# Kernel optimization log

Hardware: AMD Instinct MI355X
Metric: run time of the kernel (lower is better)

Reference implementation:

```python
import jax, jax.numpy as jnp
import numpy as np
from jax import lax

DIM = 1024
BATCH = 16
WIDTH = 2048
DECAY = 0.99


def setup_inputs() -> dict:
    key = jax.random.key(0)
    k1, k2, k3, k4 = jax.random.split(key, 4)
    scale = 1.0 / np.sqrt(DIM)
    x = jax.random.normal(k1, (BATCH, WIDTH, DIM), dtype=jnp.float32)
    state = jnp.zeros((BATCH, DIM), dtype=jnp.float32)
    Wv = jax.random.normal(k2, (DIM, DIM), dtype=jnp.float32) * scale
    Wr = jax.random.normal(k3, (DIM, DIM), dtype=jnp.float32) * scale
    Wc = jax.random.normal(k4, (DIM, DIM), dtype=jnp.float32) * scale
    return {"x": x, "state": state, "Wv": Wv, "Wr": Wr, "Wc": Wc}


def reference(x, state, Wv, Wr, Wc):
    # x: [B, W, D], state: [B, D]; fixed-decay RWKV recurrence along width.
    decay = jnp.asarray(DECAY, dtype=x.dtype)
    one_minus = jnp.asarray(1.0, dtype=x.dtype) - decay
    v = jnp.einsum('bwd,de->bwe', x, Wv)                 # value projection
    r = jax.nn.sigmoid(jnp.einsum('bwd,de->bwe', x, Wr))  # receptance

    # scan over width (time) axis: elems shaped [W, B, D]
    def step(s_prev, inp):
        v_t, r_t, x_t = inp
        s_curr = decay * s_prev + one_minus * v_t
        y_t = x_t + r_t * s_curr
        return s_curr, y_t

    elems = (jnp.swapaxes(v, 0, 1), jnp.swapaxes(r, 0, 1), jnp.swapaxes(x, 0, 1))
    new_state, y_t = lax.scan(step, state, elems)
    y = jnp.swapaxes(y_t, 0, 1)                          # [B, W, D]
    y = y + jnp.einsum('bwd,de->bwe', y, Wc)             # minimal channel mix
    return y, new_state
```

## Files before the change

kernel.cpp:

```cpp
#include <hip/hip_runtime.h>
#include <hip/hip_bf16.h>
#include <math.h>


#define MROWS 32768
#define NCHUNK 16
#define CHUNKL 128
#define DECAY_F 0.99f
#define OM_F 0.01f

typedef __attribute__((ext_vector_type(8))) short short8;
typedef __attribute__((ext_vector_type(4))) float floatx4;

using bf16 = __hip_bfloat16;
using bf162 = __hip_bfloat162;

__device__ __forceinline__ void async_copy16(const bf16* g, bf16* l) {
  __builtin_amdgcn_global_load_lds(
      (const __attribute__((address_space(1))) unsigned int*)g,
      (__attribute__((address_space(3))) unsigned int*)l, 16, 0, 0);
}

__global__ void prep_x(const float* __restrict__ X, bf16* __restrict__ Xb) {
  const int idx = blockIdx.x * 256 + threadIdx.x;
  const float4 v = ((const float4*)X)[idx];
  union { ushort4 u; bf16 h[4]; } pk;
  pk.h[0] = __float2bfloat16(v.x);
  pk.h[1] = __float2bfloat16(v.y);
  pk.h[2] = __float2bfloat16(v.z);
  pk.h[3] = __float2bfloat16(v.w);
  ((ushort4*)Xb)[idx] = pk.u;
}

__global__ void prep_weights(const float* __restrict__ Wv,
                             const float* __restrict__ Wr,
                             const float* __restrict__ Wc,
                             bf16* __restrict__ WT) {
  __shared__ float tile[32][33];
  const int bk = blockIdx.x * 32;
  const int bn = blockIdx.y * 32;
  const float* src;
  int nbase = bn;
  if (bn < 1024)      { src = Wv; }
  else if (bn < 2048) { src = Wr; nbase = bn - 1024; }
  else                { src = Wc; nbase = bn - 2048; }
  const int tx = threadIdx.x;
  const int ty = threadIdx.y;
  #pragma unroll
  for (int i = ty; i < 32; i += 8)
    tile[i][tx] = src[(size_t)(bk + i) * 1024 + nbase + tx];
  __syncthreads();
  #pragma unroll
  for (int i = ty; i < 32; i += 8)
    WT[(size_t)(bn + i) * 1024 + bk + tx] = __float2bfloat16(tile[tx][i]);
}

__global__ __launch_bounds__(256, 3) void gemm_vr(const bf16* __restrict__ Xb,
                                                  const bf16* __restrict__ WT,
                                                  bf16* __restrict__ Vout,
                                                  bf16* __restrict__ Rout) {
  __shared__ bf16 As[128][32];
  __shared__ bf16 Bs[128][32];
  const int t = threadIdx.x;
  const int id = blockIdx.x;
  const int grp = id >> 3, xcd = id & 7;
  const int mt = ((grp >> 4) << 3) | xcd;
  const int nt = grp & 15;
  const int m0 = mt * 128;
  const int lane = t & 63, wave = t >> 6;
  const int wm = wave >> 1, wn = wave & 1;
  const int ln15 = lane & 15, qd = lane >> 4;

  const bf16* Asrc = Xb + (size_t)m0 * 1024;
  const bf16* Bsrc = WT + (size_t)(nt * 128) * 1024;

  const int srow = lane >> 2;
  const int skb  = (lane & 3) * 8;

  floatx4 acc[4][4];
  #pragma unroll
  for (int i = 0; i < 4; ++i)
    #pragma unroll
    for (int j = 0; j < 4; ++j) acc[i][j] = (floatx4){0.f, 0.f, 0.f, 0.f};

  for (int k0 = 0; k0 < 1024; k0 += 32) {
    #pragma unroll
    for (int s = 0; s < 2; ++s) {
      const int seg = wave * 2 + s;
      const size_t roff = (size_t)(seg * 16 + srow) * 1024 + k0 + skb;
      async_copy16(&Asrc[roff], &As[seg * 16][0]);
      async_copy16(&Bsrc[roff], &Bs[seg * 16][0]);
    }
    __syncthreads();
    short8 fa[4], fb[4];
    #pragma unroll
    for (int tm = 0; tm < 4; ++tm)
      fa[tm] = *(const short8*)&As[wm * 64 + tm * 16 + ln15][qd * 8];
    #pragma unroll
    for (int tn = 0; tn < 4; ++tn)
      fb[tn] = *(const short8*)&Bs[wn * 64 + tn * 16 + ln15][qd * 8];
    #pragma unroll
    for (int tm = 0; tm < 4; ++tm)
      #pragma unroll
      for (int tn = 0; tn < 4; ++tn)
        acc[tm][tn] = __builtin_amdgcn_mfma_f32_16x16x32_bf16(
            fa[tm], fb[tn], acc[tm][tn], 0, 0, 0);
    __syncthreads();
  }

  const bool isr = (nt >= 8);
  bf16* outp = isr ? Rout : Vout;
  const int nc0 = (nt & 7) * 128;
  #pragma unroll
  for (int tm = 0; tm < 4; ++tm) {
    #pragma unroll
    for (int i = 0; i < 4; ++i) {
      const int m_g = m0 + wm * 64 + tm * 16 + qd * 4 + i;
      const size_t rowoff = (size_t)m_g * 1024 + nc0;
      #pragma unroll
      for (int tn = 0; tn < 4; ++tn) {
        float cv = acc[tm][tn][i];
        if (isr) cv = 1.0f / (1.0f + __expf(-cv));
        outp[rowoff + wn * 64 + tn * 16 + ln15] = __float2bfloat16(cv);
      }
    }
  }
}

__global__ void scan_partial(const bf16* __restrict__ V, float* __restrict__ sl) {
  const int idx = blockIdx.x * 256 + threadIdx.x;
  const int d2 = idx & 511;
  const int c = (idx >> 9) & 15;
  const int b = idx >> 13;
  const bf162* V2 = (const bf162*)V;
  const size_t base = (size_t)(b * 2048 + c * 128) * 512 + d2;
  float s0 = 0.f, s1 = 0.f;
  for (int w = 0; w < CHUNKL; ++w) {
    const bf162 v = V2[base + (size_t)w * 512];
    s0 = DECAY_F * s0 + OM_F * __bfloat162float(v.x);
    s1 = DECAY_F * s1 + OM_F * __bfloat162float(v.y);
  }
  const int o = (b * 16 + c) * 1024 + d2 * 2;
  sl[o] = s0;
  sl[o + 1] = s1;
}

__global__ void scan_chunk(const float* __restrict__ state,
                           const float* __restrict__ sl,
                           float* __restrict__ sin_,
                           float* __restrict__ state_out,
                           float decayL) {
  const int idx = blockIdx.x * 256 + threadIdx.x;
  const int d = idx & 1023;
  const int b = idx >> 10;
  float s = state[idx];
  #pragma unroll
  for (int c = 0; c < NCHUNK; ++c) {
    const int o = (b * 16 + c) * 1024 + d;
    sin_[o] = s;
    s = decayL * s + sl[o];
  }
  state_out[idx] = s;
}

__global__ void scan_apply(const bf16* __restrict__ Xb,
                           const bf16* __restrict__ R,
                           const float* __restrict__ sin_,
                           bf16* __restrict__ VY) {
  const int idx = blockIdx.x * 256 + threadIdx.x;
  const int d2 = idx & 511;
  const int c = (idx >> 9) & 15;
  const int b = idx >> 13;
  const bf162* R2 = (const bf162*)R;
  const bf162* X2 = (const bf162*)Xb;
  bf162* VY2 = (bf162*)VY;
  const size_t base = (size_t)(b * 2048 + c * 128) * 512 + d2;
  const int so = (b * 16 + c) * 1024 + d2 * 2;
  float s0 = sin_[so], s1 = sin_[so + 1];
  for (int w = 0; w < CHUNKL; ++w) {
    const size_t off = base + (size_t)w * 512;
    const bf162 v = VY2[off];
    const bf162 r = R2[off];
    const bf162 xx = X2[off];
    s0 = DECAY_F * s0 + OM_F * __bfloat162float(v.x);
    s1 = DECAY_F * s1 + OM_F * __bfloat162float(v.y);
    const float y0 = __bfloat162float(xx.x) + __bfloat162float(r.x) * s0;
    const float y1 = __bfloat162float(xx.y) + __bfloat162float(r.y) * s1;
    bf162 o;
    o.x = __float2bfloat16(y0);
    o.y = __float2bfloat16(y1);
    VY2[off] = o;
  }
}

__global__ __launch_bounds__(256, 3) void gemm_mix(const bf16* __restrict__ Yt,
                                                   const bf16* __restrict__ WcT,
                                                   float* __restrict__ Out) {
  __shared__ bf16 As[128][32];
  __shared__ bf16 Bs[128][32];
  const int t = threadIdx.x;
  const int id = blockIdx.x;
  const int grp = id >> 3, xcd = id & 7;
  const int mt = ((grp >> 3) << 3) | xcd;
  const int nt = grp & 7;
  const int m0 = mt * 128;
  const int nc0 = nt * 128;
  const int lane = t & 63, wave = t >> 6;
  const int wm = wave >> 1, wn = wave & 1;
  const int ln15 = lane & 15, qd = lane >> 4;

  const bf16* Asrc = Yt + (size_t)m0 * 1024;
  const bf16* Bsrc = WcT + (size_t)nc0 * 1024;

  const int srow = lane >> 2;
  const int skb  = (lane & 3) * 8;

  floatx4 acc[4][4];
  #pragma unroll
  for (int i = 0; i < 4; ++i)
    #pragma unroll
    for (int j = 0; j < 4; ++j) acc[i][j] = (floatx4){0.f, 0.f, 0.f, 0.f};

  for (int k0 = 0; k0 < 1024; k0 += 32) {
    #pragma unroll
    for (int s = 0; s < 2; ++s) {
      const int seg = wave * 2 + s;
      const size_t roff = (size_t)(seg * 16 + srow) * 1024 + k0 + skb;
      async_copy16(&Asrc[roff], &As[seg * 16][0]);
      async_copy16(&Bsrc[roff], &Bs[seg * 16][0]);
    }
    __syncthreads();
    short8 fa[4], fb[4];
    #pragma unroll
    for (int tm = 0; tm < 4; ++tm)
      fa[tm] = *(const short8*)&As[wm * 64 + tm * 16 + ln15][qd * 8];
    #pragma unroll
    for (int tn = 0; tn < 4; ++tn)
      fb[tn] = *(const short8*)&Bs[wn * 64 + tn * 16 + ln15][qd * 8];
    #pragma unroll
    for (int tm = 0; tm < 4; ++tm)
      #pragma unroll
      for (int tn = 0; tn < 4; ++tn)
        acc[tm][tn] = __builtin_amdgcn_mfma_f32_16x16x32_bf16(
            fa[tm], fb[tn], acc[tm][tn], 0, 0, 0);
    __syncthreads();
  }

  #pragma unroll
  for (int tm = 0; tm < 4; ++tm) {
    #pragma unroll
    for (int i = 0; i < 4; ++i) {
      const int m_g = m0 + wm * 64 + tm * 16 + qd * 4 + i;
      const size_t rowoff = (size_t)m_g * 1024 + nc0;
      #pragma unroll
      for (int tn = 0; tn < 4; ++tn) {
        const size_t o = rowoff + wn * 64 + tn * 16 + ln15;
        Out[o] = __bfloat162float(Yt[o]) + acc[tm][tn][i];
      }
    }
  }
}

extern "C" void kernel_launch(void* const* d_in, const int* in_sizes, int n_in,
                              void* d_out, int out_size, void* d_ws, size_t ws_size,
                              hipStream_t stream) {
  const float* x     = (const float*)d_in[0];
  const float* state = (const float*)d_in[1];
  const float* Wv    = (const float*)d_in[2];
  const float* Wr    = (const float*)d_in[3];
  const float* Wc    = (const float*)d_in[4];

  float* y_out = (float*)d_out;
  float* state_out = y_out + (size_t)MROWS * 1024;

  char* ws = (char*)d_ws;
  bf16* WT   = (bf16*)ws;
  bf16* Xb   = (bf16*)(ws + ((size_t)6 << 20));
  bf16* Vbuf = (bf16*)(ws + ((size_t)70 << 20));
  bf16* Rbuf = (bf16*)(ws + ((size_t)134 << 20));
  float* sl  = (float*)(ws + ((size_t)198 << 20));
  float* sin_ = (float*)(ws + ((size_t)199 << 20));
  bf16* WcT = WT + (size_t)2048 * 1024;

  const float decayL = (float)pow(0.99, (double)CHUNKL);

  prep_x<<<32768, 256, 0, stream>>>(x, Xb);
  prep_weights<<<dim3(32, 96), dim3(32, 8), 0, stream>>>(Wv, Wr, Wc, WT);
  gemm_vr<<<4096, 256, 0, stream>>>(Xb, WT, Vbuf, Rbuf);
  scan_partial<<<512, 256, 0, stream>>>(Vbuf, sl);
  scan_chunk<<<64, 256, 0, stream>>>(state, sl, sin_, state_out, decayL);
  scan_apply<<<512, 256, 0, stream>>>(Xb, Rbuf, sin_, Vbuf);
  gemm_mix<<<2048, 256, 0, stream>>>(Vbuf, WcT, y_out);
}
```

Measured before the change: 528.9 us.

## Replace GEMMs with 256x256-tile double-buffered, swizzled-LDS pipelined MFMA kernel

Both projection GEMMs now use one templated kernel with 256x256 tiles, 512 threads and 8x4 MFMA fragments per wave. It double-buffers LDS, interleaves async global-to-LDS loads between MFMA phases with vmcnt waits and barriers, and raises wave priority during MFMA bursts. LDS addresses are XOR-swizzled to avoid bank conflicts. The goal is to hide memory latency and cut the per-k-step sync overhead of the old 128x128 single-buffer kernels. In exchange, register pressure and code complexity rise, and the hand-coded waitcnt/barrier schedule is fragile.

```diff
diff --git a/kernel.cpp b/kernel.cpp
--- a/kernel.cpp
+++ b/kernel.cpp
@@ -15,11 +15,23 @@
 using bf16 = __hip_bfloat16;
 using bf162 = __hip_bfloat162;
 
-__device__ __forceinline__ void async_copy16(const bf16* g, bf16* l) {
+__device__ __forceinline__ void async_copy16(const void* g, void* l) {
   __builtin_amdgcn_global_load_lds(
       (const __attribute__((address_space(1))) unsigned int*)g,
       (__attribute__((address_space(3))) unsigned int*)l, 16, 0, 0);
 }
+
+#define S_BARRIER() asm volatile("s_barrier" ::: "memory")
+#define VMCNT3()                                                               \
+  do {                                                                         \
+    asm volatile("s_waitcnt vmcnt(3)" ::: "memory");                           \
+    __builtin_amdgcn_sched_barrier(0);                                         \
+  } while (0)
+#define VMCNT0()                                                               \
+  do {                                                                         \
+    asm volatile("s_waitcnt vmcnt(0)" ::: "memory");                           \
+    __builtin_amdgcn_sched_barrier(0);                                         \
+  } while (0)
 
 __global__ void prep_x(const float* __restrict__ X, bf16* __restrict__ Xb) {
   const int idx = blockIdx.x * 256 + threadIdx.x;
@@ -55,73 +67,161 @@
     WT[(size_t)(bn + i) * 1024 + bk + tx] = __float2bfloat16(tile[tx][i]);
 }
 
-__global__ __launch_bounds__(256, 3) void gemm_vr(const bf16* __restrict__ Xb,
-                                                  const bf16* __restrict__ WT,
-                                                  bf16* __restrict__ Vout,
-                                                  bf16* __restrict__ Rout) {
-  __shared__ bf16 As[128][32];
-  __shared__ bf16 Bs[128][32];
+#define PH_MFMA(M0)                                                            \
+  __builtin_amdgcn_s_setprio(1);                                               \
+  _Pragma("unroll")                                                            \
+  for (int nf = 0; nf < 4; ++nf)                                               \
+    acc[M0][nf] = __builtin_amdgcn_mfma_f32_16x16x32_bf16(                     \
+        fa[M0], fb[nf], acc[M0][nf], 0, 0, 0);                                 \
+  _Pragma("unroll")                                                            \
+  for (int nf = 0; nf < 4; ++nf)                                               \
+    acc[M0 + 1][nf] = __builtin_amdgcn_mfma_f32_16x16x32_bf16(                 \
+        fa[M0 + 1], fb[nf], acc[M0 + 1][nf], 0, 0, 0);                         \
+  __builtin_amdgcn_s_setprio(0);
+
+#define MFMA_ALL()                                                             \
+  __builtin_amdgcn_s_setprio(1);                                               \
+  _Pragma("unroll")                                                            \
+  for (int mf = 0; mf < 8; ++mf)                                               \
+    _Pragma("unroll")                                                          \
+    for (int nf = 0; nf < 4; ++nf)                                             \
+      acc[mf][nf] = __builtin_amdgcn_mfma_f32_16x16x32_bf16(                   \
+          fa[mf], fb[nf], acc[mf][nf], 0, 0, 0);                               \
+  __builtin_amdgcn_s_setprio(0);
+
+template <int MODE>
+__global__ __launch_bounds__(512, 2) void gemm8(const bf16* __restrict__ Ab,
+                                                const bf16* __restrict__ Bw,
+                                                bf16* __restrict__ Vout,
+                                                bf16* __restrict__ Rout,
+                                                float* __restrict__ Fout) {
+  __shared__ char lds[65536];
+  constexpr int NTN = (MODE == 0) ? 8 : 4;
+
+  const int nwg = gridDim.x;
+  const int id = blockIdx.x;
+  const int wg = (id & 7) * (nwg >> 3) + (id >> 3);
+  const int mt = wg / NTN, nt = wg % NTN;
+  const int m0 = mt * 256, n0 = nt * 256;
+
   const int t = threadIdx.x;
-  const int id = blockIdx.x;
-  const int grp = id >> 3, xcd = id & 7;
-  const int mt = ((grp >> 4) << 3) | xcd;
-  const int nt = grp & 15;
-  const int m0 = mt * 128;
-  const int lane = t & 63, wave = t >> 6;
-  const int wm = wave >> 1, wn = wave & 1;
-  const int ln15 = lane & 15, qd = lane >> 4;
-
-  const bf16* Asrc = Xb + (size_t)m0 * 1024;
-  const bf16* Bsrc = WT + (size_t)(nt * 128) * 1024;
-
-  const int srow = lane >> 2;
-  const int skb  = (lane & 3) * 8;
-
-  floatx4 acc[4][4];
+  const int l = t & 63, w = t >> 6;
+  const int wm = w >> 2, wn = w & 3;
+
+  const int srow = w * 16 + (l >> 2);
+  const int scol = ((l & 3) ^ ((l >> 3) & 3)) << 4;
+  const char* Abase = (const char*)Ab;
+  const char* Bbase = (const char*)Bw;
+  const char* gA0 = Abase + (size_t)(m0 + srow) * 2048 + scol;
+  const char* gA1 = gA0 + (size_t)128 * 2048;
+  const char* gB0 = Bbase + (size_t)(n0 + srow) * 2048 + scol;
+  const char* gB1 = gB0 + (size_t)128 * 2048;
+
+  const int wb = w * 1024;
+
+  const int ll = l & 15;
+  const int laneoff = ((ll * 64) + ((l >> 4) << 4)) ^ (((ll >> 1) & 3) << 4);
+
+  floatx4 acc[8][4];
   #pragma unroll
-  for (int i = 0; i < 4; ++i)
+  for (int i = 0; i < 8; ++i)
     #pragma unroll
     for (int j = 0; j < 4; ++j) acc[i][j] = (floatx4){0.f, 0.f, 0.f, 0.f};
 
-  for (int k0 = 0; k0 < 1024; k0 += 32) {
-    #pragma unroll
-    for (int s = 0; s < 2; ++s) {
-      const int seg = wave * 2 + s;
-      const size_t roff = (size_t)(seg * 16 + srow) * 1024 + k0 + skb;
-      async_copy16(&Asrc[roff], &As[seg * 16][0]);
-      async_copy16(&Bsrc[roff], &Bs[seg * 16][0]);
+  async_copy16(gB0, lds + 16384 + wb);
+  async_copy16(gB1, lds + 24576 + wb);
+  async_copy16(gA0, lds + 0 + wb);
+  async_copy16(gA1, lds + 8192 + wb);
+  async_copy16(gB0 + 64, lds + 32768 + 16384 + wb);
+  async_copy16(gB1 + 64, lds + 32768 + 24576 + wb);
+  async_copy16(gA0 + 64, lds + 32768 + 0 + wb);
+  gB0 += 128; gB1 += 128; gA0 += 128; gA1 += 64;
+  VMCNT3();
+  S_BARRIER();
+
+  short8 fa[8], fb[4];
+
+  for (int T = 0; T < 30; ++T) {
+    const int cb = (T & 1) << 15;
+    const char* smA = lds + cb + wm * 8192 + laneoff;
+    const char* smB = lds + cb + 16384 + wn * 4096 + laneoff;
+    #pragma unroll
+    for (int nf = 0; nf < 4; ++nf) fb[nf] = *(const short8*)(smB + nf * 1024);
+    #pragma unroll
+    for (int mf = 0; mf < 4; ++mf) fa[mf] = *(const short8*)(smA + mf * 1024);
+    async_copy16(gA1, lds + (cb ^ 32768) + 8192 + wb); gA1 += 64;
+    S_BARRIER();
+    PH_MFMA(0)
+    S_BARRIER();
+    #pragma unroll
+    for (int mf = 4; mf < 8; ++mf) fa[mf] = *(const short8*)(smA + mf * 1024);
+    async_copy16(gB0, lds + cb + 16384 + wb); gB0 += 64;
+    S_BARRIER();
+    PH_MFMA(2)
+    S_BARRIER();
+    async_copy16(gB1, lds + cb + 24576 + wb); gB1 += 64;
+    S_BARRIER();
+    PH_MFMA(4)
+    S_BARRIER();
+    async_copy16(gA0, lds + cb + wb); gA0 += 64;
+    S_BARRIER();
+    PH_MFMA(6)
+    VMCNT3();
+    S_BARRIER();
+  }
+
+  {
+    const char* smA = lds + wm * 8192 + laneoff;
+    const char* smB = lds + 16384 + wn * 4096 + laneoff;
+    #pragma unroll
+    for (int nf = 0; nf < 4; ++nf) fb[nf] = *(const short8*)(smB + nf * 1024);
+    #pragma unroll
+    for (int mf = 0; mf < 8; ++mf) fa[mf] = *(const short8*)(smA + mf * 1024);
+    async_copy16(gA1, lds + 32768 + 8192 + wb);
+    MFMA_ALL()
+    VMCNT0();
+    S_BARRIER();
+  }
+  {
+    const char* smA = lds + 32768 + wm * 8192 + laneoff;
+    const char* smB = lds + 32768 + 16384 + wn * 4096 + laneoff;
+    #pragma unroll
+    for (int nf = 0; nf < 4; ++nf) fb[nf] = *(const short8*)(smB + nf * 1024);
+    #pragma unroll
+    for (int mf = 0; mf < 8; ++mf) fa[mf] = *(const short8*)(smA + mf * 1024);
+    MFMA_ALL()
+  }
+
+  const int orow0 = m0 + wm * 128 + (l >> 4) * 4;
+  const int ocol = n0 + wn * 64 + ll;
+  if constexpr (MODE == 0) {
+    const bool isr = (n0 >= 1024);
+    bf16* outp = isr ? Rout : Vout;
+    const int oc = isr ? (ocol - 1024) : ocol;
+    #pragma unroll
+    for (int mf = 0; mf < 8; ++mf) {
+      #pragma unroll
+      for (int i = 0; i < 4; ++i) {
+        const size_t ro = (size_t)(orow0 + mf * 16 + i) * 1024 + oc;
+        #pragma unroll
+        for (int nf = 0; nf < 4; ++nf) {
+          float cv = acc[mf][nf][i];
+          if (isr) cv = 1.0f / (1.0f + __expf(-cv));
+          outp[ro + nf * 16] = __float2bfloat16(cv);
+        }
+      }
     }
-    __syncthreads();
-    short8 fa[4], fb[4];
-    #pragma unroll
-    for (int tm = 0; tm < 4; ++tm)
-      fa[tm] = *(const short8*)&As[wm * 64 + tm * 16 + ln15][qd * 8];
-    #pragma unroll
-    for (int tn = 0; tn < 4; ++tn)
-      fb[tn] = *(const short8*)&Bs[wn * 64 + tn * 16 + ln15][qd * 8];
-    #pragma unroll
-    for (int tm = 0; tm < 4; ++tm)
+  } else {
+    #pragma unroll
+    for (int mf = 0; mf < 8; ++mf) {
       #pragma unroll
-      for (int tn = 0; tn < 4; ++tn)
-        acc[tm][tn] = __builtin_amdgcn_mfma_f32_16x16x32_bf16(
-            fa[tm], fb[tn], acc[tm][tn], 0, 0, 0);
-    __syncthreads();
-  }
-
-  const bool isr = (nt >= 8);
-  bf16* outp = isr ? Rout : Vout;
-  const int nc0 = (nt & 7) * 128;
-  #pragma unroll
-  for (int tm = 0; tm < 4; ++tm) {
-    #pragma unroll
-    for (int i = 0; i < 4; ++i) {
-      const int m_g = m0 + wm * 64 + tm * 16 + qd * 4 + i;
-      const size_t rowoff = (size_t)m_g * 1024 + nc0;
-      #pragma unroll
-      for (int tn = 0; tn < 4; ++tn) {
-        float cv = acc[tm][tn][i];
-        if (isr) cv = 1.0f / (1.0f + __expf(-cv));
-        outp[rowoff + wn * 64 + tn * 16 + ln15] = __float2bfloat16(cv);
+      for (int i = 0; i < 4; ++i) {
+        const size_t ro = (size_t)(orow0 + mf * 16 + i) * 1024 + ocol;
+        #pragma unroll
+        for (int nf = 0; nf < 4; ++nf) {
+          const size_t o = ro + nf * 16;
+          Fout[o] = __bfloat162float(Ab[o]) + acc[mf][nf][i];
+        }
       }
     }
   }
@@ -193,74 +293,6 @@
   }
 }
 
-__global__ __launch_bounds__(256, 3) void gemm_mix(const bf16* __restrict__ Yt,
-                                                   const bf16* __restrict__ WcT,
-                                                   float* __restrict__ Out) {
-  __shared__ bf16 As[128][32];
-  __shared__ bf16 Bs[128][32];
-  const int t = threadIdx.x;
-  const int id = blockIdx.x;
-  const int grp = id >> 3, xcd = id & 7;
-  const int mt = ((grp >> 3) << 3) | xcd;
-  const int nt = grp & 7;
-  const int m0 = mt * 128;
-  const int nc0 = nt * 128;
-  const int lane = t & 63, wave = t >> 6;
-  const int wm = wave >> 1, wn = wave & 1;
-  const int ln15 = lane & 15, qd = lane >> 4;
-
-  const bf16* Asrc = Yt + (size_t)m0 * 1024;
-  const bf16* Bsrc = WcT + (size_t)nc0 * 1024;
-
-  const int srow = lane >> 2;
-  const int skb  = (lane & 3) * 8;
-
-  floatx4 acc[4][4];
-  #pragma unroll
-  for (int i = 0; i < 4; ++i)
-    #pragma unroll
-    for (int j = 0; j < 4; ++j) acc[i][j] = (floatx4){0.f, 0.f, 0.f, 0.f};
-
-  for (int k0 = 0; k0 < 1024; k0 += 32) {
-    #pragma unroll
-    for (int s = 0; s < 2; ++s) {
-      const int seg = wave * 2 + s;
-      const size_t roff = (size_t)(seg * 16 + srow) * 1024 + k0 + skb;
-      async_copy16(&Asrc[roff], &As[seg * 16][0]);
-      async_copy16(&Bsrc[roff], &Bs[seg * 16][0]);
-    }
-    __syncthreads();
-    short8 fa[4], fb[4];
-    #pragma unroll
-    for (int tm = 0; tm < 4; ++tm)
-      fa[tm] = *(const short8*)&As[wm * 64 + tm * 16 + ln15][qd * 8];
-    #pragma unroll
-    for (int tn = 0; tn < 4; ++tn)
-      fb[tn] = *(const short8*)&Bs[wn * 64 + tn * 16 + ln15][qd * 8];
-    #pragma unroll
-    for (int tm = 0; tm < 4; ++tm)
-      #pragma unroll
-      for (int tn = 0; tn < 4; ++tn)
-        acc[tm][tn] = __builtin_amdgcn_mfma_f32_16x16x32_bf16(
-            fa[tm], fb[tn], acc[tm][tn], 0, 0, 0);
-    __syncthreads();
-  }
-
-  #pragma unroll
-  for (int tm = 0; tm < 4; ++tm) {
-    #pragma unroll
-    for (int i = 0; i < 4; ++i) {
-      const int m_g = m0 + wm * 64 + tm * 16 + qd * 4 + i;
-      const size_t rowoff = (size_t)m_g * 1024 + nc0;
-      #pragma unroll
-      for (int tn = 0; tn < 4; ++tn) {
-        const size_t o = rowoff + wn * 64 + tn * 16 + ln15;
-        Out[o] = __bfloat162float(Yt[o]) + acc[tm][tn][i];
-      }
-    }
-  }
-}
-
 extern "C" void kernel_launch(void* const* d_in, const int* in_sizes, int n_in,
                               void* d_out, int out_size, void* d_ws, size_t ws_size,
                               hipStream_t stream) {
@@ -286,9 +318,9 @@
 
   prep_x<<<32768, 256, 0, stream>>>(x, Xb);
   prep_weights<<<dim3(32, 96), dim3(32, 8), 0, stream>>>(Wv, Wr, Wc, WT);
-  gemm_vr<<<4096, 256, 0, stream>>>(Xb, WT, Vbuf, Rbuf);
+  gemm8<0><<<1024, 512, 0, stream>>>(Xb, WT, Vbuf, Rbuf, nullptr);
   scan_partial<<<512, 256, 0, stream>>>(Vbuf, sl);
   scan_chunk<<<64, 256, 0, stream>>>(state, sl, sin_, state_out, decayL);
   scan_apply<<<512, 256, 0, stream>>>(Xb, Rbuf, sin_, Vbuf);
-  gemm_mix<<<2048, 256, 0, stream>>>(Vbuf, WcT, y_out);
-}
+  gemm8<1><<<512, 512, 0, stream>>>(Vbuf, WcT, nullptr, nullptr, y_out);
+}
```

Measured after the change: 515.4 us. -2.6%, faster.
